# Kernel tuning notes

Hardware: AMD Instinct MI355X
Metric: run time of the kernel (lower is better)

## Reference

```python
import jax, jax.numpy as jnp
import numpy as np

N, E = 100000, 1600000          # nodes, edges
H, DH = 8, 256                  # heads, dim_hidden
D = DH // H                     # dim per head
NEG_SLOPE = 0.2                 # GAT leaky_relu slope
BETA = 0.5


def setup_inputs() -> dict:
    key = jax.random.key(0)
    ks = jax.random.split(key, 10)
    s = 1.0 / np.sqrt(DH)
    return {
        "x": jax.random.normal(ks[0], (N, DH), jnp.float32),
        "edge_index": jax.random.randint(ks[1], (2, E), 0, N, jnp.int32),
        "edge_attr": jax.random.uniform(ks[2], (E,), jnp.float32),
        # GAT params (no bias, add_self_loops=False)
        "Wg": jax.random.normal(ks[3], (DH, DH), jnp.float32) * s,
        "att_src": jax.random.normal(ks[4], (H, D), jnp.float32) * s,
        "att_dst": jax.random.normal(ks[5], (H, D), jnp.float32) * s,
        # h_lin
        "Wh": jax.random.normal(ks[6], (DH, DH), jnp.float32) * s,
        "bh": jnp.zeros((DH,), jnp.float32),
        # lin
        "Wl": jax.random.normal(ks[7], (DH, DH), jnp.float32) * s,
        "bl": jnp.zeros((DH,), jnp.float32),
        # LayerNorm
        "ln_g": jnp.ones((DH,), jnp.float32),
        "ln_b": jnp.zeros((DH,), jnp.float32),
        # beta gate (beta>=0 -> constant vector)
        "b_param": jnp.full((DH,), BETA, jnp.float32),
    }


def _layer_norm(v, g, b, eps=1e-5):
    mu = jnp.mean(v, axis=-1, keepdims=True)
    var = jnp.var(v, axis=-1, keepdims=True)
    return (v - mu) * jax.lax.rsqrt(var + eps) * g + b


def _weighted_gat(x, edge_index, edge_attr, Wg, att_src, att_dst):
    # GATConv with per-edge weights folded into the softmax numerator.
    xs = (x @ Wg).reshape(N, H, D)                       # [N,H,D]
    a_src = jnp.einsum("nhd,hd->nh", xs, att_src)        # [N,H]
    a_dst = jnp.einsum("nhd,hd->nh", xs, att_dst)
    src, dst = edge_index[0], edge_index[1]
    e = jax.nn.leaky_relu(a_src[src] + a_dst[dst], NEG_SLOPE)   # [E,H]
    m = jax.ops.segment_max(e, dst, num_segments=N)             # [N,H]
    m = jnp.where(jnp.isfinite(m), m, 0.0)                      # isolated nodes
    p = jnp.exp(e - m[dst]) * edge_attr[:, None]                # weighted exp
    denom = jax.ops.segment_sum(p, dst, num_segments=N)         # [N,H]
    alpha = p / (denom[dst] + 1e-16)                            # [E,H]
    msg = alpha[:, :, None] * xs[src]                           # [E,H,D]
    out = jax.ops.segment_sum(msg, dst, num_segments=N)         # [N,H,D]
    return out.reshape(N, DH)


def reference(x, edge_index, edge_attr, Wg, att_src, att_dst, Wh, bh, Wl, bl, ln_g, ln_b, b_param):
    x_in = x
    h = jax.nn.relu(x @ Wh + bh)
    xg = _weighted_gat(x, edge_index, edge_attr, Wg, att_src, att_dst) + (x @ Wl + bl)
    xg = jax.nn.relu(xg)                                  # dropout p=0 (eval)
    beta = b_param[None, :]
    out = (1.0 - beta) * _layer_norm(h * xg, ln_g, ln_b) + beta * xg
    return out + x_in                                     # residual=True
```

## Files before the change

### kernel.cpp

```cpp
#include <hip/hip_runtime.h>

typedef __attribute__((ext_vector_type(4))) float f32x4;
typedef __attribute__((ext_vector_type(8))) __bf16 bf16x8;

__device__ __forceinline__ unsigned short f2bf(float f) {
    return __builtin_bit_cast(unsigned short, (__bf16)f);
}
__device__ __forceinline__ float bf2f(unsigned short u) {
    return __builtin_bit_cast(float, (unsigned)u << 16);
}

__device__ __forceinline__ void gload16(const void* g, void* l) {
    __builtin_amdgcn_global_load_lds(
        (const __attribute__((address_space(1))) void*)g,
        (__attribute__((address_space(3))) void*)l, 16, 0, 0);
}

__global__ __launch_bounds__(256) void k_cvt_x(const float* __restrict__ x,
                                               unsigned short* __restrict__ xb,
                                               long total, long totalPad) {
    long i = ((long)blockIdx.x * 256 + threadIdx.x) * 4;
    if (i >= totalPad) return;
    if (i < total) {
        float4 v = *(const float4*)(x + i);
        ushort4 u;
        u.x = f2bf(v.x); u.y = f2bf(v.y); u.z = f2bf(v.z); u.w = f2bf(v.w);
        *(ushort4*)(xb + i) = u;
    } else {
        ushort4 u = {0, 0, 0, 0};
        *(ushort4*)(xb + i) = u;
    }
}

__global__ __launch_bounds__(256) void k_wt(const float* __restrict__ Wg,
                                            const float* __restrict__ Wh,
                                            const float* __restrict__ Wl,
                                            unsigned short* __restrict__ wt) {
    int t = blockIdx.x * 256 + threadIdx.x;
    int nn = t >> 8, k = t & 255;
    const float* W = (nn < 256) ? Wg : (nn < 512) ? Wh : Wl;
    int c = nn & 255;
    wt[t] = f2bf(W[k * 256 + c]);
}

__global__ __launch_bounds__(256) void k_gemm(
    const unsigned short* __restrict__ A,
    const unsigned short* __restrict__ BT,
    unsigned short* __restrict__ xs, unsigned short* __restrict__ hb,
    unsigned short* __restrict__ xlb,
    const float* __restrict__ bh, const float* __restrict__ bl, int M) {
    __shared__ unsigned short Al[128 * 32];
    __shared__ unsigned short Bl[128 * 32];
    const int tid = threadIdx.x;
    const int lane = tid & 63;
    const int wave = tid >> 6;
    const int tm = blockIdx.x, tn = blockIdx.y;
    const int wm = (wave >> 1) * 64, wn = (wave & 1) * 64;

    f32x4 acc[4][4] = {};

    const int r0 = tid >> 2;
    const int ce = (tid & 3) * 8;
    const unsigned short* Ag = A + (size_t)tm * 128 * 256 + (size_t)r0 * 256 + ce;
    const unsigned short* Bg = BT + (size_t)tn * 128 * 256 + (size_t)r0 * 256 + ce;

    const int fr = lane & 15;
    const int ko = (lane >> 4) * 8;

    for (int ks = 0; ks < 8; ++ks) {
        const int k0 = ks * 32;
#pragma unroll
        for (int s = 0; s < 2; ++s) {
            gload16(Ag + (size_t)s * 64 * 256 + k0, (char*)Al + s * 4096 + wave * 1024);
            gload16(Bg + (size_t)s * 64 * 256 + k0, (char*)Bl + s * 4096 + wave * 1024);
        }
        __syncthreads();
        bf16x8 af[4], bfr[4];
#pragma unroll
        for (int i = 0; i < 4; ++i) {
            af[i]  = *(const bf16x8*)&Al[(wm + i * 16 + fr) * 32 + ko];
            bfr[i] = *(const bf16x8*)&Bl[(wn + i * 16 + fr) * 32 + ko];
        }
#pragma unroll
        for (int i = 0; i < 4; ++i)
#pragma unroll
            for (int j = 0; j < 4; ++j)
                acc[i][j] = __builtin_amdgcn_mfma_f32_16x16x32_bf16(af[i], bfr[j], acc[i][j], 0, 0, 0);
        __syncthreads();
    }

    const int colbase = tn * 128 + wn;
    const int rbase = tm * 128 + wm + (lane >> 4) * 4;
#pragma unroll
    for (int i = 0; i < 4; ++i) {
#pragma unroll
        for (int j = 0; j < 4; ++j) {
            const int cg = colbase + j * 16 + (lane & 15);
#pragma unroll
            for (int q = 0; q < 4; ++q) {
                const int rg = rbase + i * 16 + q;
                if (rg < M) {
                    float v = acc[i][j][q];
                    if (cg < 256) {
                        xs[(size_t)rg * 256 + cg] = f2bf(v);
                    } else if (cg < 512) {
                        float t = v + bh[cg - 256];
                        hb[(size_t)rg * 256 + (cg - 256)] = f2bf(t > 0.f ? t : 0.f);
                    } else {
                        xlb[(size_t)rg * 256 + (cg - 512)] = f2bf(v + bl[cg - 512]);
                    }
                }
            }
        }
    }
}

__global__ __launch_bounds__(256) void k_attn(const unsigned short* __restrict__ xs,
                                              const float* __restrict__ att_src,
                                              const float* __restrict__ att_dst,
                                              float* __restrict__ a_src,
                                              float* __restrict__ a_dst, int N) {
    int t = blockIdx.x * 256 + threadIdx.x;
    int n = t >> 3, hh = t & 7;
    if (n >= N) return;
    const ushort4* xp = (const ushort4*)(xs + (size_t)n * 256 + hh * 32);
    const float4* sp = (const float4*)(att_src + hh * 32);
    const float4* dp = (const float4*)(att_dst + hh * 32);
    float sa = 0.f, sd = 0.f;
#pragma unroll
    for (int q = 0; q < 8; ++q) {
        ushort4 u = xp[q];
        float4 s = sp[q], d = dp[q];
        float v0 = bf2f(u.x), v1 = bf2f(u.y), v2 = bf2f(u.z), v3 = bf2f(u.w);
        sa += v0 * s.x + v1 * s.y + v2 * s.z + v3 * s.w;
        sd += v0 * d.x + v1 * d.y + v2 * d.z + v3 * d.w;
    }
    a_src[t] = sa;
    a_dst[t] = sd;
}

__global__ void k_hist(const int* __restrict__ dst, int E, int* __restrict__ deg) {
    for (int e = blockIdx.x * blockDim.x + threadIdx.x; e < E; e += gridDim.x * blockDim.x)
        atomicAdd(&deg[dst[e]], 1);
}

__global__ __launch_bounds__(256) void k_scan1(const int* __restrict__ deg, int* __restrict__ offs,
                                               int* __restrict__ bsum, int Npad) {
    __shared__ int s[256];
    int t = threadIdx.x;
    int i = blockIdx.x * 256 + t;
    int v = (i < Npad) ? deg[i] : 0;
    s[t] = v;
    __syncthreads();
#pragma unroll
    for (int off = 1; off < 256; off <<= 1) {
        int x = (t >= off) ? s[t - off] : 0;
        __syncthreads();
        s[t] += x;
        __syncthreads();
    }
    offs[i] = s[t] - v;
    if (t == 255) bsum[blockIdx.x] = s[255];
}

__global__ __launch_bounds__(512) void k_scan2(int* __restrict__ bsum, int nb) {
    __shared__ int s[512];
    int t = threadIdx.x;
    int v = (t < nb) ? bsum[t] : 0;
    s[t] = v;
    __syncthreads();
#pragma unroll
    for (int off = 1; off < 512; off <<= 1) {
        int x = (t >= off) ? s[t - off] : 0;
        __syncthreads();
        s[t] += x;
        __syncthreads();
    }
    if (t < nb) bsum[t] = s[t] - v;
}

__global__ __launch_bounds__(256) void k_scan3(int* __restrict__ offs, const int* __restrict__ bsum,
                                               int* __restrict__ cursor) {
    int i = blockIdx.x * 256 + threadIdx.x;
    int o = offs[i] + bsum[blockIdx.x];
    offs[i] = o;
    cursor[i] = o;
}

__global__ void k_scatter(const int* __restrict__ ei, const float* __restrict__ ea, int E,
                          int* __restrict__ cursor, int* __restrict__ csr_src,
                          float* __restrict__ csr_w) {
    for (int e = blockIdx.x * blockDim.x + threadIdx.x; e < E; e += gridDim.x * blockDim.x) {
        int d = ei[(size_t)E + e];
        int pos = atomicAdd(&cursor[d], 1);
        csr_src[pos] = ei[e];
        csr_w[pos] = ea[e];
    }
}

__global__ __launch_bounds__(256) void k_agg(
    const int* __restrict__ offs, const int* __restrict__ deg,
    const int* __restrict__ csr_src, const float* __restrict__ csr_w,
    const float* __restrict__ a_src, const float* __restrict__ a_dst,
    const unsigned short* __restrict__ xs, const unsigned short* __restrict__ hb,
    const unsigned short* __restrict__ xlb,
    const float* __restrict__ x, const float* __restrict__ ln_g, const float* __restrict__ ln_b,
    const float* __restrict__ beta, float* __restrict__ out, int N) {
    const int wave = threadIdx.x >> 6, lane = threadIdx.x & 63;
    const int n = blockIdx.x * 4 + wave;
    if (n >= N) return;
    const int start = offs[n];
    const int end = start + deg[n];
    const int hM = lane >> 3;
    const float adstM = a_dst[n * 8 + hM];

    f32x4 acc = {0.f, 0.f, 0.f, 0.f};
    float denom = 0.f;
    for (int p = start; p < end; ++p) {
        int s = csr_src[p];
        float w = csr_w[p];
        float e = a_src[s * 8 + hM] + adstM;
        e = (e > 0.f) ? e : 0.2f * e;
        float pv = __expf(e) * w;
        denom += pv;
        ushort4 u = *(const ushort4*)(xs + (size_t)s * 256 + lane * 4);
        acc[0] += pv * bf2f(u.x);
        acc[1] += pv * bf2f(u.y);
        acc[2] += pv * bf2f(u.z);
        acc[3] += pv * bf2f(u.w);
    }
    const float inv = 1.f / (denom + 1e-16f);

    const size_t base = (size_t)n * 256 + lane * 4;
    ushort4 xlu = *(const ushort4*)(xlb + base);
    ushort4 hu = *(const ushort4*)(hb + base);
    f32x4 xg;
    f32x4 t4;
    float s1 = 0.f, s2 = 0.f;
    const float xl0[4] = {bf2f(xlu.x), bf2f(xlu.y), bf2f(xlu.z), bf2f(xlu.w)};
    const float hv0[4] = {bf2f(hu.x), bf2f(hu.y), bf2f(hu.z), bf2f(hu.w)};
#pragma unroll
    for (int q = 0; q < 4; ++q) {
        float g = acc[q] * inv + xl0[q];
        g = g > 0.f ? g : 0.f;
        xg[q] = g;
        float t = hv0[q] * g;
        t4[q] = t;
        s1 += t;
        s2 += t * t;
    }
#pragma unroll
    for (int off = 32; off; off >>= 1) {
        s1 += __shfl_xor(s1, off);
        s2 += __shfl_xor(s2, off);
    }
    const float mu = s1 * (1.f / 256.f);
    const float var = s2 * (1.f / 256.f) - mu * mu;
    const float rs = rsqrtf(var + 1e-5f);

    f32x4 g4 = *(const f32x4*)(ln_g + lane * 4);
    f32x4 b4 = *(const f32x4*)(ln_b + lane * 4);
    f32x4 be = *(const f32x4*)(beta + lane * 4);
    f32x4 xin = *(const f32x4*)(x + base);
    f32x4 o;
#pragma unroll
    for (int q = 0; q < 4; ++q) {
        float ln = (t4[q] - mu) * rs * g4[q] + b4[q];
        o[q] = (1.f - be[q]) * ln + be[q] * xg[q] + xin[q];
    }
    *(f32x4*)(out + base) = o;
}

extern "C" void kernel_launch(void* const* d_in, const int* in_sizes, int n_in,
                              void* d_out, int out_size, void* d_ws, size_t ws_size,
                              hipStream_t stream) {
    const float* x = (const float*)d_in[0];
    const int* ei = (const int*)d_in[1];
    const float* ea = (const float*)d_in[2];
    const float* Wg = (const float*)d_in[3];
    const float* att_src = (const float*)d_in[4];
    const float* att_dst = (const float*)d_in[5];
    const float* Wh = (const float*)d_in[6];
    const float* bh = (const float*)d_in[7];
    const float* Wl = (const float*)d_in[8];
    const float* bl = (const float*)d_in[9];
    const float* ln_g = (const float*)d_in[10];
    const float* ln_b = (const float*)d_in[11];
    const float* beta = (const float*)d_in[12];
    float* out = (float*)d_out;

    const int DH = 256;
    const int N = in_sizes[0] / DH;
    const int E = in_sizes[2];
    const int Mpad = ((N + 127) / 128) * 128;
    const int Npad = ((N + 255) / 256) * 256;
    const int nscanb = Npad / 256;

    char* w = (char*)d_ws;
    auto take = [&](size_t bytes) -> char* {
        char* p = w;
        w += (bytes + 255) & ~(size_t)255;
        return p;
    };
    unsigned short* xs = (unsigned short*)take((size_t)N * DH * 2);
    unsigned short* hb = (unsigned short*)take((size_t)N * DH * 2);
    unsigned short* xlb = (unsigned short*)take((size_t)N * DH * 2);
    float* a_src = (float*)take((size_t)N * 8 * 4);
    float* a_dst = (float*)take((size_t)N * 8 * 4);
    unsigned short* xbf = (unsigned short*)take((size_t)Mpad * DH * 2);
    unsigned short* wt = (unsigned short*)take((size_t)768 * 256 * 2);
    int* deg = (int*)take((size_t)Npad * 4);
    int* offs = (int*)take((size_t)Npad * 4);
    int* cursor = (int*)take((size_t)Npad * 4);
    int* bsum = (int*)take(512 * 4);
    int* csr_src = (int*)take((size_t)E * 4);
    float* csr_w = (float*)take((size_t)E * 4);

    hipMemsetAsync(deg, 0, (size_t)Npad * 4, stream);

    k_cvt_x<<<Mpad / 4, 256, 0, stream>>>(x, xbf, (long)N * DH, (long)Mpad * DH);
    k_wt<<<768, 256, 0, stream>>>(Wg, Wh, Wl, wt);

    k_hist<<<2048, 256, 0, stream>>>(ei + E, E, deg);
    k_scan1<<<nscanb, 256, 0, stream>>>(deg, offs, bsum, Npad);
    k_scan2<<<1, 512, 0, stream>>>(bsum, nscanb);
    k_scan3<<<nscanb, 256, 0, stream>>>(offs, bsum, cursor);
    k_scatter<<<2048, 256, 0, stream>>>(ei, ea, E, cursor, csr_src, csr_w);

    k_gemm<<<dim3(Mpad / 128, 6), 256, 0, stream>>>(xbf, wt, xs, hb, xlb, bh, bl, N);

    k_attn<<<(N * 8 + 255) / 256, 256, 0, stream>>>(xs, att_src, att_dst, a_src, a_dst, N);

    k_agg<<<(N + 3) / 4, 256, 0, stream>>>(offs, deg, csr_src, csr_w, a_src, a_dst,
                                           xs, hb, xlb, x, ln_g, ln_b, beta, out, N);
}
```

Before: 660.8 us.

## Batch edge gathers per wave, pack CSR as int2, remap GEMM blocks across XCDs

The aggregation kernel now has each group of eight lanes load eight edges at once. It computes their attention weights in parallel and broadcasts sources and weights with shuffles, so eight independent row gathers are in flight instead of one serial dependent chain. The CSR source and weight arrays are merged into one int2 array, so each edge needs a single load. The GEMM launch is flattened into a 1D grid with an XCD-aware block remap so adjacent tiles share each chiplet's L2. The cost is wasted lanes on low-degree nodes and more register pressure from the eight buffered rows.

```diff
diff --git a/kernel.cpp b/kernel.cpp
--- a/kernel.cpp
+++ b/kernel.cpp
@@ -48,13 +48,18 @@
     const unsigned short* __restrict__ BT,
     unsigned short* __restrict__ xs, unsigned short* __restrict__ hb,
     unsigned short* __restrict__ xlb,
-    const float* __restrict__ bh, const float* __restrict__ bl, int M) {
+    const float* __restrict__ bh, const float* __restrict__ bl, int M, int nwg) {
     __shared__ unsigned short Al[128 * 32];
     __shared__ unsigned short Bl[128 * 32];
+    const int bid = blockIdx.x;
+    const int xcd = bid & 7, idx = bid >> 3;
+    const int q = nwg >> 3, r = nwg & 7;
+    const int wg = (xcd < r ? xcd * (q + 1) : r * (q + 1) + (xcd - r) * q) + idx;
+    const int tm = wg / 6, tn = wg % 6;
+
     const int tid = threadIdx.x;
     const int lane = tid & 63;
     const int wave = tid >> 6;
-    const int tm = blockIdx.x, tn = blockIdx.y;
     const int wm = (wave >> 1) * 64, wn = (wave & 1) * 64;
 
     f32x4 acc[4][4] = {};
@@ -97,10 +102,10 @@
         for (int j = 0; j < 4; ++j) {
             const int cg = colbase + j * 16 + (lane & 15);
 #pragma unroll
-            for (int q = 0; q < 4; ++q) {
-                const int rg = rbase + i * 16 + q;
+            for (int q2 = 0; q2 < 4; ++q2) {
+                const int rg = rbase + i * 16 + q2;
                 if (rg < M) {
-                    float v = acc[i][j][q];
+                    float v = acc[i][j][q2];
                     if (cg < 256) {
                         xs[(size_t)rg * 256 + cg] = f2bf(v);
                     } else if (cg < 512) {
@@ -188,19 +193,20 @@
 }
 
 __global__ void k_scatter(const int* __restrict__ ei, const float* __restrict__ ea, int E,
-                          int* __restrict__ cursor, int* __restrict__ csr_src,
-                          float* __restrict__ csr_w) {
+                          int* __restrict__ cursor, int2* __restrict__ csr) {
     for (int e = blockIdx.x * blockDim.x + threadIdx.x; e < E; e += gridDim.x * blockDim.x) {
         int d = ei[(size_t)E + e];
         int pos = atomicAdd(&cursor[d], 1);
-        csr_src[pos] = ei[e];
-        csr_w[pos] = ea[e];
+        int2 sw;
+        sw.x = ei[e];
+        sw.y = __builtin_bit_cast(int, ea[e]);
+        csr[pos] = sw;
     }
 }
 
 __global__ __launch_bounds__(256) void k_agg(
     const int* __restrict__ offs, const int* __restrict__ deg,
-    const int* __restrict__ csr_src, const float* __restrict__ csr_w,
+    const int2* __restrict__ csr,
     const float* __restrict__ a_src, const float* __restrict__ a_dst,
     const unsigned short* __restrict__ xs, const unsigned short* __restrict__ hb,
     const unsigned short* __restrict__ xlb,
@@ -210,41 +216,62 @@
     const int n = blockIdx.x * 4 + wave;
     if (n >= N) return;
     const int start = offs[n];
-    const int end = start + deg[n];
-    const int hM = lane >> 3;
-    const float adstM = a_dst[n * 8 + hM];
+    const int dcount = deg[n];
+    const int head = lane >> 3;
+    const int eSub = lane & 7;
+    const float adst = a_dst[n * 8 + head];
 
     f32x4 acc = {0.f, 0.f, 0.f, 0.f};
-    float denom = 0.f;
-    for (int p = start; p < end; ++p) {
-        int s = csr_src[p];
-        float w = csr_w[p];
-        float e = a_src[s * 8 + hM] + adstM;
-        e = (e > 0.f) ? e : 0.2f * e;
-        float pv = __expf(e) * w;
-        denom += pv;
-        ushort4 u = *(const ushort4*)(xs + (size_t)s * 256 + lane * 4);
-        acc[0] += pv * bf2f(u.x);
-        acc[1] += pv * bf2f(u.y);
-        acc[2] += pv * bf2f(u.z);
-        acc[3] += pv * bf2f(u.w);
-    }
-    const float inv = 1.f / (denom + 1e-16f);
+    float dsum = 0.f;
+    const unsigned short* xrow = xs + (size_t)lane * 4;
+
+    for (int g = 0; g < dcount; g += 8) {
+        const int eIdx = g + eSub;
+        int src = 0;
+        float w = 0.f;
+        if (eIdx < dcount) {
+            int2 sw = csr[start + eIdx];
+            src = sw.x;
+            w = __builtin_bit_cast(float, sw.y);
+        }
+        float a = a_src[src * 8 + head] + adst;
+        a = (a > 0.f) ? a : 0.2f * a;
+        const float pv = __expf(a) * w;
+        dsum += pv;
+
+        ushort4 rows[8];
+#pragma unroll
+        for (int e = 0; e < 8; ++e) {
+            const int s = __shfl(src, e);
+            rows[e] = *(const ushort4*)(xrow + (size_t)s * 256);
+        }
+#pragma unroll
+        for (int e = 0; e < 8; ++e) {
+            const float p = __shfl(pv, (lane & 56) + e);
+            acc[0] += p * bf2f(rows[e].x);
+            acc[1] += p * bf2f(rows[e].y);
+            acc[2] += p * bf2f(rows[e].z);
+            acc[3] += p * bf2f(rows[e].w);
+        }
+    }
+    dsum += __shfl_xor(dsum, 1);
+    dsum += __shfl_xor(dsum, 2);
+    dsum += __shfl_xor(dsum, 4);
+    const float inv = 1.f / (dsum + 1e-16f);
 
     const size_t base = (size_t)n * 256 + lane * 4;
     ushort4 xlu = *(const ushort4*)(xlb + base);
     ushort4 hu = *(const ushort4*)(hb + base);
-    f32x4 xg;
-    f32x4 t4;
+    f32x4 xg, t4;
     float s1 = 0.f, s2 = 0.f;
     const float xl0[4] = {bf2f(xlu.x), bf2f(xlu.y), bf2f(xlu.z), bf2f(xlu.w)};
     const float hv0[4] = {bf2f(hu.x), bf2f(hu.y), bf2f(hu.z), bf2f(hu.w)};
 #pragma unroll
     for (int q = 0; q < 4; ++q) {
-        float g = acc[q] * inv + xl0[q];
-        g = g > 0.f ? g : 0.f;
-        xg[q] = g;
-        float t = hv0[q] * g;
+        float gg = acc[q] * inv + xl0[q];
+        gg = gg > 0.f ? gg : 0.f;
+        xg[q] = gg;
+        float t = hv0[q] * gg;
         t4[q] = t;
         s1 += t;
         s2 += t * t;
@@ -295,6 +322,7 @@
     const int Mpad = ((N + 127) / 128) * 128;
     const int Npad = ((N + 255) / 256) * 256;
     const int nscanb = Npad / 256;
+    const int nwg = (Mpad / 128) * 6;
 
     char* w = (char*)d_ws;
     auto take = [&](size_t bytes) -> char* {
@@ -313,8 +341,7 @@
     int* offs = (int*)take((size_t)Npad * 4);
     int* cursor = (int*)take((size_t)Npad * 4);
     int* bsum = (int*)take(512 * 4);
-    int* csr_src = (int*)take((size_t)E * 4);
-    float* csr_w = (float*)take((size_t)E * 4);
+    int2* csr = (int2*)take((size_t)E * 8);
 
     hipMemsetAsync(deg, 0, (size_t)Npad * 4, stream);
 
@@ -325,12 +352,12 @@
     k_scan1<<<nscanb, 256, 0, stream>>>(deg, offs, bsum, Npad);
     k_scan2<<<1, 512, 0, stream>>>(bsum, nscanb);
     k_scan3<<<nscanb, 256, 0, stream>>>(offs, bsum, cursor);
-    k_scatter<<<2048, 256, 0, stream>>>(ei, ea, E, cursor, csr_src, csr_w);
-
-    k_gemm<<<dim3(Mpad / 128, 6), 256, 0, stream>>>(xbf, wt, xs, hb, xlb, bh, bl, N);
+    k_scatter<<<2048, 256, 0, stream>>>(ei, ea, E, cursor, csr);
+
+    k_gemm<<<nwg, 256, 0, stream>>>(xbf, wt, xs, hb, xlb, bh, bl, N, nwg);
 
     k_attn<<<(N * 8 + 255) / 256, 256, 0, stream>>>(xs, att_src, att_dst, a_src, a_dst, N);
 
-    k_agg<<<(N + 3) / 4, 256, 0, stream>>>(offs, deg, csr_src, csr_w, a_src, a_dst,
+    k_agg<<<(N + 3) / 4, 256, 0, stream>>>(offs, deg, csr, a_src, a_dst,
                                            xs, hb, xlb, x, ln_g, ln_b, beta, out, N);
 }
```

New measurement: 585.2 us. -11.4%, faster.
